# Kernel optimization log

Hardware: AMD Instinct MI355X
Metric: run time of the kernel (lower is better)

The kernel has to match this reference:

```python
import jax, jax.numpy as jnp
import numpy as np

DIM = 1024
HEADS = 16
DIM_HEAD = 64
INNER = HEADS * DIM_HEAD  # 1024
SCALE = DIM ** (-0.5)  # module scales by dim**-0.5 (not dim_head)


def setup_inputs() -> dict:
    key = jax.random.key(0)
    kx, kqkv, kwo, kbo = jax.random.split(key, 4)
    x = jax.random.normal(kx, (2, 2048, DIM), dtype=jnp.float32)
    W_qkv = jax.random.normal(kqkv, (DIM, 3 * INNER), dtype=jnp.float32) * (DIM ** -0.5)
    W_out = jax.random.normal(kwo, (INNER, DIM), dtype=jnp.float32) * (INNER ** -0.5)
    b_out = jax.random.normal(kbo, (DIM,), dtype=jnp.float32) * 0.01
    return {"x": x, "W_qkv": W_qkv, "W_out": W_out, "b_out": b_out}


def reference(x, W_qkv, W_out, b_out):
    b, n, _ = x.shape
    qkv = x @ W_qkv  # [b, n, 3*inner]
    q, k, v = jnp.split(qkv, 3, axis=-1)
    # [b, n, h*d] -> [b, h, n, d]
    reshape = lambda t: t.reshape(b, n, HEADS, DIM_HEAD).transpose(0, 2, 1, 3)
    q, k, v = reshape(q), reshape(k), reshape(v)
    dots = jnp.einsum('bhid,bhjd->bhij', q, k) * SCALE  # [b, h, n, n]
    attn = jax.nn.softmax(dots, axis=-1)
    out = jnp.einsum('bhij,bhjd->bhid', attn, v)  # [b, h, n, d]
    out = out.transpose(0, 2, 1, 3).reshape(b, n, INNER)
    return out @ W_out + b_out
```

## Files before the change

### kernel.cpp

```cpp
#include <hip/hip_runtime.h>

typedef __bf16 bf16x8 __attribute__((ext_vector_type(8)));
typedef __bf16 bf16x4 __attribute__((ext_vector_type(4)));
typedef float f32x4 __attribute__((ext_vector_type(4)));
typedef float f32x16 __attribute__((ext_vector_type(16)));

__device__ __forceinline__ void async16(void* lds, const void* g) {
  __builtin_amdgcn_global_load_lds(
      (__attribute__((address_space(1))) unsigned int*)(g),
      (__attribute__((address_space(3))) unsigned int*)(lds), 16, 0, 0);
}

__device__ __forceinline__ int detect_block(const unsigned short* win, int* cnt_sh) {
  if (threadIdx.x == 0) *cnt_sh = 0;
  __syncthreads();
  int c = 0;
#pragma unroll
  for (int j = 0; j < 8; j++) {
    const unsigned short u = win[threadIdx.x * 8 + j];
    if (((u >> 7) & 0xFF) >= 0xC0) c++;
  }
  if (c) atomicAdd(cnt_sh, c);
  __syncthreads();
  return (*cnt_sh >= 64) ? 1 : 0;
}

__global__ __launch_bounds__(256) void prep(
    const void* __restrict__ x, const void* __restrict__ Wqkv,
    const void* __restrict__ Wout, __bf16* __restrict__ xb,
    __bf16* __restrict__ WqkvT, __bf16* __restrict__ WoutT,
    int* __restrict__ flagp)
{
  __shared__ __bf16 tile[64 * 65];
  __shared__ int cnt;
  const int bx = blockIdx.x;
  const int t = threadIdx.x;

  if (bx < 2048) {
    const long base = (long)bx * 2048;
    const int f = detect_block((const unsigned short*)x + base, &cnt);
    if (bx == 0 && t == 0) *flagp = f;
    const long i = base + t * 8;
    if (f) {
      const float* s = (const float*)x;
#pragma unroll
      for (int j = 0; j < 8; j++) xb[i + j] = (__bf16)s[i + j];
    } else {
      *(bf16x8*)&xb[i] = *(const bf16x8*)((const __bf16*)x + i);
    }
    return;
  }

  const void* in;  __bf16* out;  int R = 1024, C, tcx, tr;
  if (bx < 2816) {
    const int idx = bx - 2048;
    in = Wqkv; out = WqkvT; C = 3072; tcx = (idx % 48) * 64; tr = (idx / 48) * 64;
  } else {
    const int idx = bx - 2816;
    in = Wout; out = WoutT; C = 1024; tcx = (idx % 16) * 64; tr = (idx / 16) * 64;
  }
  const int f = detect_block((const unsigned short*)in + (long)tr * C + tcx, &cnt);
#pragma unroll
  for (int i = 0; i < 16; i++) {
    const int idx = t + 256 * i;
    const int r = idx >> 6, c = idx & 63;
    const long g = (long)(tr + r) * C + tcx + c;
    tile[r * 65 + c] = f ? (__bf16)((const float*)in)[g] : ((const __bf16*)in)[g];
  }
  __syncthreads();
#pragma unroll
  for (int i = 0; i < 16; i++) {
    const int idx = t + 256 * i;
    const int r = idx >> 6, c = idx & 63;
    out[(long)(tcx + r) * R + tr + c] = tile[c * 65 + r];
  }
}

__global__ __launch_bounds__(256, 3) void gemm_qkv(
    const __bf16* __restrict__ A, const __bf16* __restrict__ Bt,
    __bf16* __restrict__ Cqk, __bf16* __restrict__ Vt)
{
  __shared__ __bf16 smem[17408];
  const int t = threadIdx.x;
  const int l = t & 63;
  const int w = t >> 6;
  const int wr = w >> 1, wc = w & 1;
  const long m0 = (long)blockIdx.x * 128;
  const long n0 = (long)blockIdx.y * 128;
  const int K = 1024;

  const int srow = w * 16 + (l >> 2);
  const int skof = (l & 3) * 8;
  const __bf16* gA = A + (m0 + srow) * (long)K + skof;
  const __bf16* gB = Bt + (n0 + srow) * (long)K + skof;
  const int Ao[2] = {0, 8192}, Bo[2] = {4096, 12288};
  const int lof = w * 512 + l * 8;

  async16(smem + Ao[0] + lof,        gA);
  async16(smem + Ao[0] + 2048 + lof, gA + 64 * (long)K);
  async16(smem + Bo[0] + lof,        gB);
  async16(smem + Bo[0] + 2048 + lof, gB + 64 * (long)K);
  gA += 32; gB += 32;
  __syncthreads();

  f32x4 acc[4][4] = {};

  for (int it = 0; it < 32; it++) {
    if (it < 31) {
      const int nb = (it + 1) & 1;
      async16(smem + Ao[nb] + lof,        gA);
      async16(smem + Ao[nb] + 2048 + lof, gA + 64 * (long)K);
      async16(smem + Bo[nb] + lof,        gB);
      async16(smem + Bo[nb] + 2048 + lof, gB + 64 * (long)K);
      gA += 32; gB += 32;
    }
    const __bf16* As = smem + Ao[it & 1];
    const __bf16* Bs = smem + Bo[it & 1];
    bf16x8 af[4], bfr[4];
#pragma unroll
    for (int mi = 0; mi < 4; mi++)
      af[mi] = *(const bf16x8*)&As[(wr * 64 + mi * 16 + (l & 15)) * 32 + (l >> 4) * 8];
#pragma unroll
    for (int ni = 0; ni < 4; ni++)
      bfr[ni] = *(const bf16x8*)&Bs[(wc * 64 + ni * 16 + (l & 15)) * 32 + (l >> 4) * 8];
#pragma unroll
    for (int mi = 0; mi < 4; mi++)
#pragma unroll
      for (int ni = 0; ni < 4; ni++)
        acc[mi][ni] = __builtin_amdgcn_mfma_f32_16x16x32_bf16(af[mi], bfr[ni], acc[mi][ni], 0, 0, 0);
    __syncthreads();
  }

  if (n0 < 2048) {
#pragma unroll
    for (int mi = 0; mi < 4; mi++)
#pragma unroll
      for (int ni = 0; ni < 4; ni++) {
        const long col = n0 + wc * 64 + ni * 16 + (l & 15);
#pragma unroll
        for (int r = 0; r < 4; r++) {
          const long row = m0 + wr * 64 + mi * 16 + (l >> 4) * 4 + r;
          Cqk[row * 2048 + col] = (__bf16)acc[mi][ni][r];
        }
      }
  } else {
#pragma unroll
    for (int mi = 0; mi < 4; mi++)
#pragma unroll
      for (int ni = 0; ni < 4; ni++) {
        const int c = wc * 64 + ni * 16 + (l & 15);
        const int r = wr * 64 + mi * 16 + (l >> 4) * 4;
        bf16x4 pk;
#pragma unroll
        for (int k = 0; k < 4; k++) pk[k] = (__bf16)acc[mi][ni][k];
        *(bf16x4*)&smem[c * 136 + r] = pk;
      }
    __syncthreads();
    const int b = (int)(m0 >> 11);
    const int nbase = (int)(m0 & 2047);
#pragma unroll
    for (int i = 0; i < 8; i++) {
      const int c = (t >> 4) + i * 16;
      const int r8 = (t & 15) * 8;
      const bf16x8 v = *(const bf16x8*)&smem[c * 136 + r8];
      const int vcol = (int)(n0 - 2048) + c;
      *(bf16x8*)&Vt[((long)(b * 16 + (vcol >> 6)) * 64 + (vcol & 63)) * 2048 + nbase + r8] = v;
    }
  }
}

__global__ __launch_bounds__(256, 2) void gemm_out(
    const __bf16* __restrict__ A, const __bf16* __restrict__ Bt,
    const void* __restrict__ bias_raw, void* __restrict__ C,
    const int* __restrict__ flagp)
{
  __shared__ __bf16 smem[12288];
  const int t = threadIdx.x;
  const int l = t & 63;
  const int w = t >> 6;
  const int wr = w >> 1, wc = w & 1;
  const long m0 = (long)blockIdx.x * 128;
  const long n0 = (long)blockIdx.y * 64;
  const int of = *flagp;
  const int K = 1024;

  const int srow = w * 16 + (l >> 2);
  const int skof = (l & 3) * 8;
  const __bf16* gA = A + (m0 + srow) * (long)K + skof;
  const __bf16* gB = Bt + (n0 + srow) * (long)K + skof;
  const int Ao[2] = {0, 6144}, Bo[2] = {4096, 10240};
  const int lof = w * 512 + l * 8;

  async16(smem + Ao[0] + lof,        gA);
  async16(smem + Ao[0] + 2048 + lof, gA + 64 * (long)K);
  async16(smem + Bo[0] + lof,        gB);
  gA += 32; gB += 32;
  __syncthreads();

  f32x4 acc[4][2] = {};

  for (int it = 0; it < 32; it++) {
    if (it < 31) {
      const int nb = (it + 1) & 1;
      async16(smem + Ao[nb] + lof,        gA);
      async16(smem + Ao[nb] + 2048 + lof, gA + 64 * (long)K);
      async16(smem + Bo[nb] + lof,        gB);
      gA += 32; gB += 32;
    }
    const __bf16* As = smem + Ao[it & 1];
    const __bf16* Bs = smem + Bo[it & 1];
    bf16x8 af[4], bfr[2];
#pragma unroll
    for (int mi = 0; mi < 4; mi++)
      af[mi] = *(const bf16x8*)&As[(wr * 64 + mi * 16 + (l & 15)) * 32 + (l >> 4) * 8];
#pragma unroll
    for (int ni = 0; ni < 2; ni++)
      bfr[ni] = *(const bf16x8*)&Bs[(wc * 32 + ni * 16 + (l & 15)) * 32 + (l >> 4) * 8];
#pragma unroll
    for (int mi = 0; mi < 4; mi++)
#pragma unroll
      for (int ni = 0; ni < 2; ni++)
        acc[mi][ni] = __builtin_amdgcn_mfma_f32_16x16x32_bf16(af[mi], bfr[ni], acc[mi][ni], 0, 0, 0);
    __syncthreads();
  }

#pragma unroll
  for (int mi = 0; mi < 4; mi++)
#pragma unroll
    for (int ni = 0; ni < 2; ni++) {
      const long col = n0 + wc * 32 + ni * 16 + (l & 15);
      const float bv = of ? ((const float*)bias_raw)[col]
                          : (float)((const __bf16*)bias_raw)[col];
#pragma unroll
      for (int r = 0; r < 4; r++) {
        const long row = m0 + wr * 64 + mi * 16 + (l >> 4) * 4 + r;
        const float val = acc[mi][ni][r] + bv;
        const long off = row * 1024 + col;
        if (of) ((float*)C)[off] = val;
        else    ((__bf16*)C)[off] = (__bf16)val;
      }
    }
}

#define EXP2_SCALE 0.045084439f

__global__ __launch_bounds__(256, 4) void attn_kernel(
    const __bf16* __restrict__ qk, const __bf16* __restrict__ Vt,
    __bf16* __restrict__ O)
{
  __shared__ __bf16 smem[20480];
  const int t = threadIdx.x;
  const int l = t & 63;
  const int w = t >> 6;
  const int wi = w & 1, wj = w >> 1;
  const int hl = l >> 5;
  const int i7 = l & 7;
  const int qt = blockIdx.x;
  const int bh = blockIdx.y;
  const int b = bh >> 4, head = bh & 15;
  const long q_row0 = (long)b * 2048 + qt * 64;

  const int srow = w * 8 + (l >> 3);
  const int sdof = ((l & 7) ^ (l >> 3)) * 8;
  const int lof = w * 512 + l * 8;
  const int Ko[2] = {4096, 12288}, Vo[2] = {8192, 16384};

  {
    const __bf16* g = qk + (q_row0 + srow) * 2048 + head * 64 + sdof;
    async16(smem + lof,        g);
    async16(smem + 2048 + lof, g + (long)32 * 2048);
  }
  const __bf16* gK = qk + ((long)b * 2048 + srow) * 2048 + 1024 + head * 64 + sdof;
  const __bf16* gV = Vt + ((long)bh * 64 + srow) * 2048 + sdof;
  async16(smem + Ko[0] + lof,        gK);
  async16(smem + Ko[0] + 2048 + lof, gK + 32 * 2048);
  async16(smem + Vo[0] + lof,        gV);
  async16(smem + Vo[0] + 2048 + lof, gV + 32 * 2048);
  gK += (long)64 * 2048;
  gV += 64;
  __syncthreads();

  bf16x8 qf[4];
#pragma unroll
  for (int kc = 0; kc < 4; kc++)
    qf[kc] = *(const bf16x8*)&smem[(wi * 32 + (l & 31)) * 64 + (((kc * 2 + hl) ^ i7) * 8)];

  f32x16 acc[2] = {};
  float l_i = 0.0f;

  for (int it = 0; it < 32; it++) {
    if (it < 31) {
      const int nb = (it + 1) & 1;
      async16(smem + Ko[nb] + lof,        gK);
      async16(smem + Ko[nb] + 2048 + lof, gK + 32 * 2048);
      async16(smem + Vo[nb] + lof,        gV);
      async16(smem + Vo[nb] + 2048 + lof, gV + 32 * 2048);
      gK += (long)64 * 2048;
      gV += 64;
    }
    const __bf16* Ks = smem + Ko[it & 1];
    const __bf16* Vs = smem + Vo[it & 1];

    f32x16 st = {0,0,0,0,0,0,0,0,0,0,0,0,0,0,0,0};
#pragma unroll
    for (int kc = 0; kc < 4; kc++) {
      const bf16x8 ak = *(const bf16x8*)&Ks[(wj * 32 + (l & 31)) * 64 + (((kc * 2 + hl) ^ i7) * 8)];
      st = __builtin_amdgcn_mfma_f32_32x32x16_bf16(ak, qf[kc], st, 0, 0, 0);
    }

    float rs = 0.0f;
#pragma unroll
    for (int r = 0; r < 16; r++) {
      const float p = exp2f(st[r] * EXP2_SCALE);
      st[r] = p;
      rs += p;
    }
    rs += __shfl_xor(rs, 32, 64);
    l_i += rs;

    unsigned pw[8], qw[8];
#pragma unroll
    for (int k2 = 0; k2 < 8; k2++) {
      union { __bf16 h2[2]; unsigned u; } cv;
      cv.h2[0] = (__bf16)st[2 * k2];
      cv.h2[1] = (__bf16)st[2 * k2 + 1];
      pw[k2] = cv.u;
    }
#pragma unroll
    for (int k2 = 0; k2 < 8; k2++)
      qw[k2] = (unsigned)__shfl_xor((int)pw[k2], 32, 64);

#pragma unroll
    for (int m = 0; m < 2; m++) {
      union { unsigned u[4]; bf16x8 v; } fa;
      fa.u[0] = hl ? qw[4 * m + 2] : pw[4 * m + 0];
      fa.u[1] = hl ? qw[4 * m + 3] : pw[4 * m + 1];
      fa.u[2] = hl ? pw[4 * m + 2] : qw[4 * m + 0];
      fa.u[3] = hl ? pw[4 * m + 3] : qw[4 * m + 1];
#pragma unroll
      for (int nd = 0; nd < 2; nd++) {
        const bf16x8 bv = *(const bf16x8*)&Vs[(nd * 32 + (l & 31)) * 64 + (((4 * wj + 2 * m + hl) ^ i7) * 8)];
        acc[nd] = __builtin_amdgcn_mfma_f32_32x32x16_bf16(fa.v, bv, acc[nd], 0, 0, 0);
      }
    }
    __syncthreads();
  }

  float* sc = (float*)(smem + 4096);
  float* lb = (float*)(smem + 12288);
  if (l < 32) lb[w * 32 + l] = l_i;
  if (wj == 1) {
#pragma unroll
    for (int nd = 0; nd < 2; nd++)
#pragma unroll
      for (int r = 0; r < 16; r++)
        sc[wi * 2048 + nd * 1024 + (int)l * 16 + r] = acc[nd][r];
  }
  __syncthreads();
  if (wj == 0) {
#pragma unroll
    for (int r = 0; r < 16; r++) {
      const int iloc = (r & 3) + 8 * (r >> 2) + 4 * hl;
      const float lt = lb[wi * 32 + iloc] + lb[(wi + 2) * 32 + iloc];
      const long row = q_row0 + wi * 32 + iloc;
#pragma unroll
      for (int nd = 0; nd < 2; nd++) {
        const float o = acc[nd][r] + sc[wi * 2048 + nd * 1024 + (int)l * 16 + r];
        O[row * 1024 + head * 64 + nd * 32 + (l & 31)] = (__bf16)(o / lt);
      }
    }
  }
}

extern "C" void kernel_launch(void* const* d_in, const int* in_sizes, int n_in,
                              void* d_out, int out_size, void* d_ws, size_t ws_size,
                              hipStream_t stream) {
  const void* x    = d_in[0];
  const void* Wqkv = d_in[1];
  const void* Wout = d_in[2];
  const void* bout = d_in[3];

  char* ws = (char*)d_ws;
  int*    flagp = (int*)ws;
  __bf16* xb    = (__bf16*)(ws + 4096);
  __bf16* WqkvT = (__bf16*)(ws + 4096 +  8388608);
  __bf16* WoutT = (__bf16*)(ws + 4096 + 14680064);
  __bf16* qkbuf = (__bf16*)(ws + 4096 + 16777216);
  __bf16* VtBuf = (__bf16*)(ws + 4096 + 33554432);
  __bf16* Obuf  = (__bf16*)(ws + 4096 + 41943040);

  hipLaunchKernelGGL(prep, dim3(3072), dim3(256), 0, stream,
                     x, Wqkv, Wout, xb, WqkvT, WoutT, flagp);
  hipLaunchKernelGGL(gemm_qkv, dim3(32, 24), dim3(256), 0, stream,
                     xb, WqkvT, qkbuf, VtBuf);
  hipLaunchKernelGGL(attn_kernel, dim3(32, 32), dim3(256), 0, stream,
                     qkbuf, VtBuf, Obuf);
  hipLaunchKernelGGL(gemm_out, dim3(32, 16), dim3(256), 0, stream,
                     Obuf, WoutT, bout, d_out, flagp);
}
```

Before: 212.9 us.

## Stage P through LDS so each wave owns a disjoint PV output tile

The attention kernel now writes the exponentiated scores P to shared memory and has each wave compute a distinct 32x32 slice of the output, instead of splitting the key dimension across waves and reducing partial accumulators through LDS at the end. This removes the cross-lane shuffles and the final LDS reduction, and halves the accumulator registers. In exchange it adds an extra barrier per iteration. The block index is also remapped so concurrently running blocks are spread across heads and batches, and the O buffer reuses the x workspace.

```diff
diff --git a/kernel.cpp b/kernel.cpp
--- a/kernel.cpp
+++ b/kernel.cpp
@@ -255,8 +255,9 @@
   const int wi = w & 1, wj = w >> 1;
   const int hl = l >> 5;
   const int i7 = l & 7;
-  const int qt = blockIdx.x;
-  const int bh = blockIdx.y;
+  const int L = blockIdx.y * 32 + blockIdx.x;
+  const int bh = (L & 7) * 4 + ((L >> 3) & 3);
+  const int qt = L >> 5;
   const int b = bh >> 4, head = bh & 15;
   const long q_row0 = (long)b * 2048 + qt * 64;
 
@@ -285,10 +286,46 @@
   for (int kc = 0; kc < 4; kc++)
     qf[kc] = *(const bf16x8*)&smem[(wi * 32 + (l & 31)) * 64 + (((kc * 2 + hl) ^ i7) * 8)];
 
-  f32x16 acc[2] = {};
+  __bf16* Ps = smem;
+  f32x16 acc = {0,0,0,0,0,0,0,0,0,0,0,0,0,0,0,0};
   float l_i = 0.0f;
 
   for (int it = 0; it < 32; it++) {
+    __syncthreads();
+    const __bf16* Ks = smem + Ko[it & 1];
+    const __bf16* Vs = smem + Vo[it & 1];
+
+    f32x16 st = {0,0,0,0,0,0,0,0,0,0,0,0,0,0,0,0};
+#pragma unroll
+    for (int kc = 0; kc < 4; kc++) {
+      const bf16x8 ak = *(const bf16x8*)&Ks[(wj * 32 + (l & 31)) * 64 + (((kc * 2 + hl) ^ i7) * 8)];
+      st = __builtin_amdgcn_mfma_f32_32x32x16_bf16(ak, qf[kc], st, 0, 0, 0);
+    }
+
+    float rs = 0.0f;
+#pragma unroll
+    for (int r = 0; r < 16; r++) {
+      const float p = exp2f(st[r] * EXP2_SCALE);
+      st[r] = p;
+      rs += p;
+    }
+    rs += __shfl_xor(rs, 32, 64);
+    l_i += rs;
+
+    {
+      const int ibase = (wi * 32 + (l & 31)) * 64;
+      const int sub = 4 * hl;
+#pragma unroll
+      for (int q = 0; q < 4; q++) {
+        bf16x4 pk;
+#pragma unroll
+        for (int r = 0; r < 4; r++) pk[r] = (__bf16)st[q * 4 + r];
+        const int gj = 4 * wj + q;
+        *(bf16x4*)&Ps[ibase + ((gj ^ i7) * 8) + sub] = pk;
+      }
+    }
+    __syncthreads();
+
     if (it < 31) {
       const int nb = (it + 1) & 1;
       async16(smem + Ko[nb] + lof,        gK);
@@ -298,77 +335,27 @@
       gK += (long)64 * 2048;
       gV += 64;
     }
-    const __bf16* Ks = smem + Ko[it & 1];
-    const __bf16* Vs = smem + Vo[it & 1];
-
-    f32x16 st = {0,0,0,0,0,0,0,0,0,0,0,0,0,0,0,0};
+
 #pragma unroll
     for (int kc = 0; kc < 4; kc++) {
-      const bf16x8 ak = *(const bf16x8*)&Ks[(wj * 32 + (l & 31)) * 64 + (((kc * 2 + hl) ^ i7) * 8)];
-      st = __builtin_amdgcn_mfma_f32_32x32x16_bf16(ak, qf[kc], st, 0, 0, 0);
-    }
-
-    float rs = 0.0f;
-#pragma unroll
-    for (int r = 0; r < 16; r++) {
-      const float p = exp2f(st[r] * EXP2_SCALE);
-      st[r] = p;
-      rs += p;
-    }
-    rs += __shfl_xor(rs, 32, 64);
-    l_i += rs;
-
-    unsigned pw[8], qw[8];
-#pragma unroll
-    for (int k2 = 0; k2 < 8; k2++) {
-      union { __bf16 h2[2]; unsigned u; } cv;
-      cv.h2[0] = (__bf16)st[2 * k2];
-      cv.h2[1] = (__bf16)st[2 * k2 + 1];
-      pw[k2] = cv.u;
-    }
-#pragma unroll
-    for (int k2 = 0; k2 < 8; k2++)
-      qw[k2] = (unsigned)__shfl_xor((int)pw[k2], 32, 64);
-
-#pragma unroll
-    for (int m = 0; m < 2; m++) {
-      union { unsigned u[4]; bf16x8 v; } fa;
-      fa.u[0] = hl ? qw[4 * m + 2] : pw[4 * m + 0];
-      fa.u[1] = hl ? qw[4 * m + 3] : pw[4 * m + 1];
-      fa.u[2] = hl ? pw[4 * m + 2] : qw[4 * m + 0];
-      fa.u[3] = hl ? pw[4 * m + 3] : qw[4 * m + 1];
-#pragma unroll
-      for (int nd = 0; nd < 2; nd++) {
-        const bf16x8 bv = *(const bf16x8*)&Vs[(nd * 32 + (l & 31)) * 64 + (((4 * wj + 2 * m + hl) ^ i7) * 8)];
-        acc[nd] = __builtin_amdgcn_mfma_f32_32x32x16_bf16(fa.v, bv, acc[nd], 0, 0, 0);
-      }
-    }
-    __syncthreads();
-  }
-
-  float* sc = (float*)(smem + 4096);
+      const int swz = ((kc * 2 + hl) ^ i7) * 8;
+      const bf16x8 ap = *(const bf16x8*)&Ps[(wi * 32 + (l & 31)) * 64 + swz];
+      const bf16x8 bv = *(const bf16x8*)&Vs[(wj * 32 + (l & 31)) * 64 + swz];
+      acc = __builtin_amdgcn_mfma_f32_32x32x16_bf16(ap, bv, acc, 0, 0, 0);
+    }
+  }
+
+  __syncthreads();
   float* lb = (float*)(smem + 12288);
   if (l < 32) lb[w * 32 + l] = l_i;
-  if (wj == 1) {
-#pragma unroll
-    for (int nd = 0; nd < 2; nd++)
-#pragma unroll
-      for (int r = 0; r < 16; r++)
-        sc[wi * 2048 + nd * 1024 + (int)l * 16 + r] = acc[nd][r];
-  }
-  __syncthreads();
-  if (wj == 0) {
-#pragma unroll
-    for (int r = 0; r < 16; r++) {
-      const int iloc = (r & 3) + 8 * (r >> 2) + 4 * hl;
-      const float lt = lb[wi * 32 + iloc] + lb[(wi + 2) * 32 + iloc];
-      const long row = q_row0 + wi * 32 + iloc;
-#pragma unroll
-      for (int nd = 0; nd < 2; nd++) {
-        const float o = acc[nd][r] + sc[wi * 2048 + nd * 1024 + (int)l * 16 + r];
-        O[row * 1024 + head * 64 + nd * 32 + (l & 31)] = (__bf16)(o / lt);
-      }
-    }
+  __syncthreads();
+#pragma unroll
+  for (int r = 0; r < 16; r++) {
+    const int iloc = (r & 3) + 8 * (r >> 2) + 4 * hl;
+    const float lt = lb[wi * 32 + iloc] + lb[(wi + 2) * 32 + iloc];
+    const long row = q_row0 + wi * 32 + iloc;
+    const long col = (long)head * 64 + wj * 32 + (l & 31);
+    O[row * 1024 + col] = (__bf16)(acc[r] / lt);
   }
 }
 
@@ -383,11 +370,11 @@
   char* ws = (char*)d_ws;
   int*    flagp = (int*)ws;
   __bf16* xb    = (__bf16*)(ws + 4096);
+  __bf16* Obuf  = xb;
   __bf16* WqkvT = (__bf16*)(ws + 4096 +  8388608);
   __bf16* WoutT = (__bf16*)(ws + 4096 + 14680064);
   __bf16* qkbuf = (__bf16*)(ws + 4096 + 16777216);
   __bf16* VtBuf = (__bf16*)(ws + 4096 + 33554432);
-  __bf16* Obuf  = (__bf16*)(ws + 4096 + 41943040);
 
   hipLaunchKernelGGL(prep, dim3(3072), dim3(256), 0, stream,
                      x, Wqkv, Wout, xb, WqkvT, WoutT, flagp);
```

Result: faster. 200.6 us (-5.8%).
